# Kernel optimization log

Hardware: AMD Instinct MI355X
Metric: run time of the kernel (lower is better)

## Reference

```python
import jax, jax.numpy as jnp
import numpy as np

N_NODES = 100000
N_EDGES = 1600000
IN_DIM = 64
HID = 128
N_GRAPHS = 64
N_CLASSES = 2
EPS = 1e-5


def setup_inputs() -> dict:
    key = jax.random.key(0)
    ks = jax.random.split(key, 8)
    x = jax.random.normal(ks[0], (N_NODES, IN_DIM), dtype=jnp.float32)
    edge_index = jax.random.randint(ks[1], (2, N_EDGES), 0, N_NODES, dtype=jnp.int64)
    batch = jnp.sort(jax.random.randint(ks[2], (N_NODES,), 0, N_GRAPHS, dtype=jnp.int64))
    W1 = jax.random.normal(ks[3], (IN_DIM, HID), dtype=jnp.float32) / np.sqrt(IN_DIM)
    b1 = jnp.zeros((HID,), jnp.float32)
    W2 = jax.random.normal(ks[4], (HID, HID), dtype=jnp.float32) / np.sqrt(HID)
    b2 = jnp.zeros((HID,), jnp.float32)
    gamma = jnp.ones((HID,), jnp.float32)
    beta = jnp.zeros((HID,), jnp.float32)
    fcW = jax.random.normal(ks[5], (HID, N_CLASSES), dtype=jnp.float32) / np.sqrt(HID)
    fcb = jnp.zeros((N_CLASSES,), jnp.float32)
    return {"x": x, "edge_index": edge_index, "batch": batch, "W1": W1, "b1": b1,
            "W2": W2, "b2": b2, "gamma": gamma, "beta": beta, "fcW": fcW, "fcb": fcb}


def reference(x, edge_index, batch, W1, b1, W2, b2, gamma, beta, fcW, fcb):
    n = x.shape[0]
    loop = jnp.arange(n)
    # GCNConv adds self-loops and uses symmetric normalization D^-1/2 (A+I) D^-1/2
    src = jnp.concatenate([edge_index[0], loop])
    dst = jnp.concatenate([edge_index[1], loop])
    deg = jax.ops.segment_sum(jnp.ones_like(dst, dtype=x.dtype), dst, num_segments=n)
    dis = jax.lax.rsqrt(deg)  # deg >= 1 thanks to self-loops
    enorm = dis[src] * dis[dst]  # [E+N]

    def gcn(h, W, b):
        h = h @ W                                   # transform first (PyG order)
        msg = h[src] * enorm[:, None]               # gather + scale
        return jax.ops.segment_sum(msg, dst, num_segments=n) + b  # scatter-add

    cnt = jnp.maximum(jax.ops.segment_sum(jnp.ones((n,), x.dtype), batch,
                                          num_segments=N_GRAPHS), 1.0)[:, None]

    def inst_norm(h):
        # per-graph, per-channel normalization over nodes (affine=False)
        mean = jax.ops.segment_sum(h, batch, num_segments=N_GRAPHS) / cnt
        var = jax.ops.segment_sum(h * h, batch, num_segments=N_GRAPHS) / cnt - mean * mean
        return (h - mean[batch]) * jax.lax.rsqrt(var[batch] + EPS)

    h = jax.nn.relu(inst_norm(gcn(x, W1, b1)))   # dropout = identity (eval)
    h = jax.nn.relu(inst_norm(gcn(h, W2, b2)))
    pooled = jax.ops.segment_sum(h, batch, num_segments=N_GRAPHS) / cnt  # global mean pool
    # BatchNorm1d over the graph dimension (batch statistics, affine)
    m = jnp.mean(pooled, axis=0)
    v = jnp.mean((pooled - m) ** 2, axis=0)
    z = (pooled - m) * jax.lax.rsqrt(v + EPS) * gamma + beta
    return z @ fcW + fcb
```

## Files before the change

kernel.cpp:

```cpp
#include <hip/hip_runtime.h>
#include <hip/hip_bf16.h>


#define HID 128
#define NGRAPH 64
#define EPSN 1e-5f
#define BSHIFT 8
#define NBMAX 512

typedef unsigned int uint;
typedef unsigned short ushort;
typedef __attribute__((ext_vector_type(8))) short short8;
typedef __attribute__((ext_vector_type(4))) float f32x4;

static __device__ __forceinline__ ushort f2bf(float f) {
  uint x = __float_as_uint(f);
  return (ushort)((x + 0x7FFFu + ((x >> 16) & 1u)) >> 16);
}
static __device__ __forceinline__ float bf_lo(uint u) { return __uint_as_float(u << 16); }
static __device__ __forceinline__ float bf_hi(uint u) {
  return __uint_as_float(u & 0xFFFF0000u);
}

__global__ __launch_bounds__(256) void graph_starts(const int* __restrict__ batch,
                                                    int* __restrict__ gstart, int N) {
  int i = blockIdx.x * 256 + threadIdx.x;
  if (i >= N) return;
  int g = batch[i];
  if (i == 0) {
    for (int q = 0; q <= g; ++q) gstart[q] = 0;
  } else {
    int gp = batch[i - 1];
    if (g != gp)
      for (int q = gp + 1; q <= g; ++q) gstart[q] = i;
  }
  if (i == N - 1)
    for (int q = g + 1; q <= NGRAPH; ++q) gstart[q] = N;
}

__global__ __launch_bounds__(256) void bin_edges(const int* __restrict__ src,
                                                 const int* __restrict__ dst,
                                                 int* __restrict__ gcursor,
                                                 uint* __restrict__ records, int E, int NB,
                                                 int cap) {
  __shared__ int h[NBMAX];
  __shared__ int base[NBMAX];
  for (int i = threadIdx.x; i < NB; i += 256) h[i] = 0;
  __syncthreads();
  int e0 = blockIdx.x * 4096;
  int d[16], s[16];
#pragma unroll
  for (int k = 0; k < 16; ++k) {
    int e = e0 + k * 256 + threadIdx.x;
    if (e < E) {
      d[k] = dst[e];
      s[k] = src[e];
      atomicAdd(&h[d[k] >> BSHIFT], 1);
    }
  }
  __syncthreads();
  for (int i = threadIdx.x; i < NB; i += 256) {
    int c = h[i];
    if (c) base[i] = i * cap + atomicAdd(&gcursor[i], c);
  }
  __syncthreads();
  for (int i = threadIdx.x; i < NB; i += 256) h[i] = 0;
  __syncthreads();
#pragma unroll
  for (int k = 0; k < 16; ++k) {
    int e = e0 + k * 256 + threadIdx.x;
    if (e < E) {
      int b = d[k] >> BSHIFT;
      int lp = atomicAdd(&h[b], 1);
      records[base[b] + lp] = ((uint)s[k] << 8) | (uint)(d[k] & 255);
    }
  }
}

__global__ __launch_bounds__(256) void build_csr(const uint* __restrict__ records,
                                                 const int* __restrict__ gcursor,
                                                 int* __restrict__ row_beg,
                                                 int* __restrict__ row_end,
                                                 float* __restrict__ dis,
                                                 int* __restrict__ esrc, int N, int cap) {
  const int b = blockIdx.x;
  const int node0 = b << BSHIFT;
  const int nn = min(256, N - node0);
  const int beg = b * cap;
  const int cnt = gcursor[b];
  const int t = threadIdx.x;
  __shared__ int lc[256], sc[256], lcur[256];
  lc[t] = 0;
  __syncthreads();
  for (int i = t; i < cnt; i += 256) atomicAdd(&lc[records[beg + i] & 255u], 1);
  __syncthreads();
  int myc = lc[t];
  sc[t] = myc;
  __syncthreads();
  for (int off = 1; off < 256; off <<= 1) {
    int add = (t >= off) ? sc[t - off] : 0;
    __syncthreads();
    sc[t] += add;
    __syncthreads();
  }
  int excl = sc[t] - myc;
  if (t < nn) {
    row_beg[node0 + t] = beg + excl;
    row_end[node0 + t] = beg + excl + myc;
    dis[node0 + t] = rsqrtf((float)myc + 1.0f);
  }
  lcur[t] = excl;
  __syncthreads();
  for (int i = t; i < cnt; i += 256) {
    uint r = records[beg + i];
    int p = atomicAdd(&lcur[r & 255u], 1);
    esrc[beg + p] = (int)(r >> 8);
  }
}

__global__ __launch_bounds__(256) void xscale_bf16(const float* __restrict__ X,
                                                   const float* __restrict__ dis,
                                                   ushort* __restrict__ XS, int n4) {
  int i4 = blockIdx.x * 256 + threadIdx.x;
  if (i4 >= n4) return;
  int n = i4 >> 4;
  float dn = dis[n];
  float4 v = ((const float4*)X)[i4];
  ushort4 u;
  u.x = f2bf(v.x * dn);
  u.y = f2bf(v.y * dn);
  u.z = f2bf(v.z * dn);
  u.w = f2bf(v.w * dn);
  ((ushort4*)XS)[i4] = u;
}

__global__ __launch_bounds__(256) void wt_both(const float* __restrict__ W1,
                                               const float* __restrict__ W2,
                                               ushort* __restrict__ w1t,
                                               ushort* __restrict__ w2t) {
  int i = blockIdx.x * 256 + threadIdx.x;
  if (i < 128 * 64) {
    int c = i / 64, k = i - c * 64;
    w1t[i] = f2bf(W1[(size_t)k * HID + c]);
  } else {
    int i2 = i - 128 * 64;
    if (i2 < 128 * 128) {
      int c = i2 / 128, k = i2 - c * 128;
      w2t[i2] = f2bf(W2[(size_t)k * HID + c]);
    }
  }
}

__global__ __launch_bounds__(256) void aggregate64(const ushort* __restrict__ XS,
                                                   const int* __restrict__ row_beg,
                                                   const int* __restrict__ row_end,
                                                   const int* __restrict__ esrc,
                                                   const float* __restrict__ dis,
                                                   ushort* __restrict__ out, int N) {
  int wave = (int)((blockIdx.x * 256 + threadIdx.x) >> 6);
  const int l = threadIdx.x & 63;
  const int n = wave * 2 + (l >> 5);
  if (n >= N) return;
  const int j = l & 31;
  const float dn = dis[n];
  const int beg = row_beg[n];
  const int len = row_end[n] - beg;
  const uint* Xj = (const uint*)XS + j;
  float a0 = 0.f, a1 = 0.f, b0 = 0.f, b1 = 0.f;
  int i = 0;
  for (; i + 7 < len; i += 8) {
    int s0 = esrc[beg + i], s1 = esrc[beg + i + 1];
    int s2 = esrc[beg + i + 2], s3 = esrc[beg + i + 3];
    int s4 = esrc[beg + i + 4], s5 = esrc[beg + i + 5];
    int s6 = esrc[beg + i + 6], s7 = esrc[beg + i + 7];
    uint u0 = Xj[(size_t)s0 * 32];
    uint u1 = Xj[(size_t)s1 * 32];
    uint u2 = Xj[(size_t)s2 * 32];
    uint u3 = Xj[(size_t)s3 * 32];
    uint u4 = Xj[(size_t)s4 * 32];
    uint u5 = Xj[(size_t)s5 * 32];
    uint u6 = Xj[(size_t)s6 * 32];
    uint u7 = Xj[(size_t)s7 * 32];
    a0 += bf_lo(u0) + bf_lo(u1) + bf_lo(u2) + bf_lo(u3);
    a1 += bf_hi(u0) + bf_hi(u1) + bf_hi(u2) + bf_hi(u3);
    b0 += bf_lo(u4) + bf_lo(u5) + bf_lo(u6) + bf_lo(u7);
    b1 += bf_hi(u4) + bf_hi(u5) + bf_hi(u6) + bf_hi(u7);
  }
  for (; i < len; ++i) {
    uint u = Xj[(size_t)esrc[beg + i] * 32];
    a0 += bf_lo(u);
    a1 += bf_hi(u);
  }
  uint us = Xj[(size_t)n * 32];
  a0 += b0 + bf_lo(us);
  a1 += b1 + bf_hi(us);
  ((uint*)out)[(size_t)n * 32 + j] = (uint)f2bf(a0 * dn) | ((uint)f2bf(a1 * dn) << 16);
}

__global__ __launch_bounds__(256) void aggregate128(const ushort* __restrict__ H,
                                                    const int* __restrict__ row_beg,
                                                    const int* __restrict__ row_end,
                                                    const int* __restrict__ esrc,
                                                    const float* __restrict__ dis,
                                                    const float* __restrict__ bias,
                                                    ushort* __restrict__ outz, int N) {
  int wave = (int)((blockIdx.x * 256 + threadIdx.x) >> 6);
  const int l = threadIdx.x & 63;
  const int n = wave * 2 + (l >> 5);
  if (n >= N) return;
  const int j = l & 31;
  const float dn = dis[n];
  const int beg = row_beg[n];
  const int len = row_end[n] - beg;
  const uint2* Hj = (const uint2*)H + j;
  float a0 = 0.f, a1 = 0.f, a2 = 0.f, a3 = 0.f;
  float b0 = 0.f, b1 = 0.f, b2 = 0.f, b3 = 0.f;
  int i = 0;
  for (; i + 7 < len; i += 8) {
    int s0 = esrc[beg + i], s1 = esrc[beg + i + 1];
    int s2 = esrc[beg + i + 2], s3 = esrc[beg + i + 3];
    int s4 = esrc[beg + i + 4], s5 = esrc[beg + i + 5];
    int s6 = esrc[beg + i + 6], s7 = esrc[beg + i + 7];
    uint2 u0 = Hj[(size_t)s0 * 32];
    uint2 u1 = Hj[(size_t)s1 * 32];
    uint2 u2 = Hj[(size_t)s2 * 32];
    uint2 u3 = Hj[(size_t)s3 * 32];
    uint2 u4 = Hj[(size_t)s4 * 32];
    uint2 u5 = Hj[(size_t)s5 * 32];
    uint2 u6 = Hj[(size_t)s6 * 32];
    uint2 u7 = Hj[(size_t)s7 * 32];
    a0 += bf_lo(u0.x) + bf_lo(u1.x) + bf_lo(u2.x) + bf_lo(u3.x);
    a1 += bf_hi(u0.x) + bf_hi(u1.x) + bf_hi(u2.x) + bf_hi(u3.x);
    a2 += bf_lo(u0.y) + bf_lo(u1.y) + bf_lo(u2.y) + bf_lo(u3.y);
    a3 += bf_hi(u0.y) + bf_hi(u1.y) + bf_hi(u2.y) + bf_hi(u3.y);
    b0 += bf_lo(u4.x) + bf_lo(u5.x) + bf_lo(u6.x) + bf_lo(u7.x);
    b1 += bf_hi(u4.x) + bf_hi(u5.x) + bf_hi(u6.x) + bf_hi(u7.x);
    b2 += bf_lo(u4.y) + bf_lo(u5.y) + bf_lo(u6.y) + bf_lo(u7.y);
    b3 += bf_hi(u4.y) + bf_hi(u5.y) + bf_hi(u6.y) + bf_hi(u7.y);
  }
  for (; i < len; ++i) {
    uint2 u = Hj[(size_t)esrc[beg + i] * 32];
    a0 += bf_lo(u.x);
    a1 += bf_hi(u.x);
    a2 += bf_lo(u.y);
    a3 += bf_hi(u.y);
  }
  uint2 us = Hj[(size_t)n * 32];
  a0 += b0 + bf_lo(us.x);
  a1 += b1 + bf_hi(us.x);
  a2 += b2 + bf_lo(us.y);
  a3 += b3 + bf_hi(us.y);
  float4 bv = ((const float4*)bias)[j];
  uint2 o;
  o.x = (uint)f2bf(a0 * dn + bv.x) | ((uint)f2bf(a1 * dn + bv.y) << 16);
  o.y = (uint)f2bf(a2 * dn + bv.z) | ((uint)f2bf(a3 * dn + bv.w) << 16);
  ((uint2*)outz)[(size_t)n * 32 + j] = o;
}

template <int K, bool FUSE_NORM, bool DIS_SCALE, bool HAS_BIAS>
__global__ __launch_bounds__(256) void gemm_mfma(const ushort* __restrict__ X,
                                                 const ushort* __restrict__ Wt,
                                                 const float* __restrict__ bias,
                                                 const int* __restrict__ batch,
                                                 const float* __restrict__ mean,
                                                 const float* __restrict__ inv,
                                                 const float* __restrict__ disv,
                                                 ushort* __restrict__ Y, int N) {
  const int t = threadIdx.x;
  const int w = t >> 6;
  const int l = t & 63;
  const int lr = l & 15;
  const int lk = l >> 4;
  const int row0 = blockIdx.x * 64 + w * 16;
  const int arow = min(row0 + lr, N - 1);
  int g = 0;
  if (FUSE_NORM) g = batch[arow];
  f32x4 acc[8];
#pragma unroll
  for (int i = 0; i < 8; ++i) acc[i] = (f32x4){0.f, 0.f, 0.f, 0.f};
#pragma unroll
  for (int k0 = 0; k0 < K; k0 += 32) {
    const int kbase = k0 + lk * 8;
    short8 a = *(const short8*)(X + (size_t)arow * K + kbase);
    if (FUSE_NORM) {
      const float* mp = mean + g * HID + kbase;
      const float* ip = inv + g * HID + kbase;
      short8 an;
#pragma unroll
      for (int j = 0; j < 8; ++j) {
        float f = __uint_as_float((uint)(ushort)a[j] << 16);
        f = fmaxf((f - mp[j]) * ip[j], 0.f);
        an[j] = (short)f2bf(f);
      }
      a = an;
    }
#pragma unroll
    for (int nf = 0; nf < 8; ++nf) {
      short8 b = *(const short8*)(Wt + (size_t)(nf * 16 + lr) * K + kbase);
      acc[nf] = __builtin_amdgcn_mfma_f32_16x16x32_bf16(a, b, acc[nf], 0, 0, 0);
    }
  }
#pragma unroll
  for (int r = 0; r < 4; ++r) {
    int grow = row0 + lk * 4 + r;
    if (grow < N) {
      float ds = DIS_SCALE ? disv[grow] : 1.f;
#pragma unroll
      for (int nf = 0; nf < 8; ++nf) {
        int col = nf * 16 + lr;
        float v = acc[nf][r];
        if (HAS_BIAS) v += bias[col];
        v *= ds;
        Y[(size_t)grow * HID + col] = f2bf(v);
      }
    }
  }
}

__global__ __launch_bounds__(256) void stats_pass(const ushort* __restrict__ G,
                                                  const int* __restrict__ batch,
                                                  float* __restrict__ gsum,
                                                  float* __restrict__ gsq, int N) {
  const int c2 = threadIdx.x & 63;
  const int sub = threadIdx.x >> 6;
  const int n0 = blockIdx.x * 64 + sub * 16;
  const int n1 = min(n0 + 16, N);
  const uint* Gj = (const uint*)G + c2;
  float s0 = 0.f, s1 = 0.f, q0 = 0.f, q1 = 0.f;
  int cur = -1;
  for (int n = n0; n < n1; ++n) {
    int g = batch[n];
    if (g != cur) {
      if (cur >= 0) {
        atomicAdd(&gsum[cur * HID + 2 * c2], s0);
        atomicAdd(&gsum[cur * HID + 2 * c2 + 1], s1);
        atomicAdd(&gsq[cur * HID + 2 * c2], q0);
        atomicAdd(&gsq[cur * HID + 2 * c2 + 1], q1);
      }
      cur = g;
      s0 = s1 = q0 = q1 = 0.f;
    }
    uint u = Gj[(size_t)n * 64];
    float v0 = bf_lo(u), v1 = bf_hi(u);
    s0 += v0;
    s1 += v1;
    q0 += v0 * v0;
    q1 += v1 * v1;
  }
  if (cur >= 0) {
    atomicAdd(&gsum[cur * HID + 2 * c2], s0);
    atomicAdd(&gsum[cur * HID + 2 * c2 + 1], s1);
    atomicAdd(&gsq[cur * HID + 2 * c2], q0);
    atomicAdd(&gsq[cur * HID + 2 * c2 + 1], q1);
  }
}

__global__ __launch_bounds__(256) void finalize_stats(const float* __restrict__ gsum,
                                                      const float* __restrict__ gsq,
                                                      const int* __restrict__ gstart,
                                                      float* __restrict__ mean,
                                                      float* __restrict__ inv) {
  int i = blockIdx.x * 256 + threadIdx.x;
  if (i >= NGRAPH * HID) return;
  int g = i >> 7;
  float c = fmaxf((float)(gstart[g + 1] - gstart[g]), 1.f);
  float m = gsum[i] / c;
  float v = gsq[i] / c - m * m;
  mean[i] = m;
  inv[i] = rsqrtf(v + EPSN);
}

__global__ __launch_bounds__(256) void norm_relu_pool(const ushort* __restrict__ G,
                                                      const int* __restrict__ batch,
                                                      const float* __restrict__ mean,
                                                      const float* __restrict__ inv,
                                                      float* __restrict__ pooled, int N) {
  const int c2 = threadIdx.x & 63;
  const int sub = threadIdx.x >> 6;
  const int n0 = blockIdx.x * 64 + sub * 16;
  const int n1 = min(n0 + 16, N);
  const uint* Gj = (const uint*)G + c2;
  float p0 = 0.f, p1 = 0.f;
  int cur = -1;
  float2 mv = {0.f, 0.f}, iv = {0.f, 0.f};
  for (int n = n0; n < n1; ++n) {
    int g = batch[n];
    if (g != cur) {
      if (cur >= 0) {
        atomicAdd(&pooled[cur * HID + 2 * c2], p0);
        atomicAdd(&pooled[cur * HID + 2 * c2 + 1], p1);
      }
      cur = g;
      p0 = p1 = 0.f;
      mv = ((const float2*)mean)[g * 64 + c2];
      iv = ((const float2*)inv)[g * 64 + c2];
    }
    uint u = Gj[(size_t)n * 64];
    p0 += fmaxf((bf_lo(u) - mv.x) * iv.x, 0.f);
    p1 += fmaxf((bf_hi(u) - mv.y) * iv.y, 0.f);
  }
  if (cur >= 0) {
    atomicAdd(&pooled[cur * HID + 2 * c2], p0);
    atomicAdd(&pooled[cur * HID + 2 * c2 + 1], p1);
  }
}

__global__ __launch_bounds__(256) void final_head(const float* __restrict__ pooled_sum,
                                                  const int* __restrict__ gstart,
                                                  const float* __restrict__ gamma,
                                                  const float* __restrict__ beta,
                                                  const float* __restrict__ fcW,
                                                  const float* __restrict__ fcb,
                                                  float* __restrict__ out) {
  __shared__ float P[NGRAPH][HID];
  __shared__ float zs[HID], zb[HID];
  int t = threadIdx.x;
  for (int i = t; i < NGRAPH * HID; i += 256) {
    int g = i >> 7;
    float c = fmaxf((float)(gstart[g + 1] - gstart[g]), 1.f);
    P[g][i & 127] = pooled_sum[i] / c;
  }
  __syncthreads();
  if (t < HID) {
    float m = 0.f;
    for (int g = 0; g < NGRAPH; ++g) m += P[g][t];
    m *= (1.f / NGRAPH);
    float v = 0.f;
    for (int g = 0; g < NGRAPH; ++g) {
      float d = P[g][t] - m;
      v += d * d;
    }
    v *= (1.f / NGRAPH);
    float sc = rsqrtf(v + EPSN) * gamma[t];
    zs[t] = sc;
    zb[t] = beta[t] - m * sc;
  }
  __syncthreads();
  if (t < NGRAPH * 2) {
    int g = t >> 1, k = t & 1;
    float acc = fcb[k];
    for (int c = 0; c < HID; ++c) {
      float z = P[g][c] * zs[c] + zb[c];
      acc += z * fcW[c * 2 + k];
    }
    out[t] = acc;
  }
}

extern "C" void kernel_launch(void* const* d_in, const int* in_sizes, int n_in,
                              void* d_out, int out_size, void* d_ws, size_t ws_size,
                              hipStream_t stream) {
  const float* x = (const float*)d_in[0];
  const int* ei = (const int*)d_in[1];
  const int* batch = (const int*)d_in[2];
  const float* W1 = (const float*)d_in[3];
  const float* b1 = (const float*)d_in[4];
  const float* W2 = (const float*)d_in[5];
  const float* b2 = (const float*)d_in[6];
  const float* gamma = (const float*)d_in[7];
  const float* beta = (const float*)d_in[8];
  const float* fcW = (const float*)d_in[9];
  const float* fcb = (const float*)d_in[10];
  float* out = (float*)d_out;

  const int N = in_sizes[2];
  const int E = in_sizes[1] / 2;
  const int* srcp = ei;
  const int* dstp = ei + E;
  const int NB = (N + 255) >> BSHIFT;
  const int cap = 2 * (E / NB) + 256;

  float* ws = (float*)d_ws;
  size_t off = 0;
  auto alloc = [&](size_t n) {
    float* p = ws + off;
    off += (n + 127) & ~(size_t)127;
    return p;
  };
  int* row_beg = (int*)alloc(N);
  int* row_end = (int*)alloc(N);
  int* esrc = (int*)alloc((size_t)NB * cap);
  size_t recsz = ((size_t)NB * cap > (size_t)N * 32 ? (size_t)NB * cap : (size_t)N * 32);
  float* recbuf = alloc(recsz);
  float* dis = alloc(N);
  float* y1b = alloc((size_t)N * 32);
  float* h1b = alloc((size_t)N * 64);
  float* h2b = alloc((size_t)N * 64);
  float* zb_ = alloc((size_t)N * 64);
  float* w1tb = alloc(128 * 64 / 2);
  float* w2tb = alloc(128 * 128 / 2);
  int* gstart = (int*)alloc(NGRAPH + 1);
  float* zero0 = ws + off;
  int* gcursor = (int*)alloc(NBMAX);
  float* gsum1 = alloc(NGRAPH * HID);
  float* gsq1 = alloc(NGRAPH * HID);
  float* gsum2 = alloc(NGRAPH * HID);
  float* gsq2 = alloc(NGRAPH * HID);
  float* pooled = alloc(NGRAPH * HID);
  size_t zero_bytes = (size_t)((ws + off) - zero0) * sizeof(float);
  float* mean1 = alloc(NGRAPH * HID);
  float* inv1 = alloc(NGRAPH * HID);
  float* mean2 = alloc(NGRAPH * HID);
  float* inv2 = alloc(NGRAPH * HID);

  uint* records = (uint*)recbuf;
  ushort* xs = (ushort*)recbuf;
  ushort* y1 = (ushort*)y1b;
  ushort* h1 = (ushort*)h1b;
  ushort* h2s = (ushort*)h2b;
  ushort* z = (ushort*)zb_;
  ushort* w1t = (ushort*)w1tb;
  ushort* w2t = (ushort*)w2tb;

  const int nblkN = (N + 255) / 256;
  const int nblkE4k = (E + 4095) / 4096;

  hipMemsetAsync(zero0, 0, zero_bytes, stream);

  wt_both<<<(128 * 64 + 128 * 128 + 255) / 256, 256, 0, stream>>>(W1, W2, w1t, w2t);
  graph_starts<<<nblkN, 256, 0, stream>>>(batch, gstart, N);
  bin_edges<<<nblkE4k, 256, 0, stream>>>(srcp, dstp, gcursor, records, E, NB, cap);
  build_csr<<<NB, 256, 0, stream>>>(records, gcursor, row_beg, row_end, dis, esrc, N, cap);

  const int aggBlocks = ((N + 1) / 2 + 3) / 4;
  const int gemmBlocks = (N + 63) / 64;
  const int nrmBlocks = (N + 63) / 64;

  xscale_bf16<<<(N * 16 + 255) / 256, 256, 0, stream>>>(x, dis, xs, N * 16);
  aggregate64<<<aggBlocks, 256, 0, stream>>>(xs, row_beg, row_end, esrc, dis, y1, N);
  gemm_mfma<64, false, false, true><<<gemmBlocks, 256, 0, stream>>>(
      y1, w1t, b1, nullptr, nullptr, nullptr, nullptr, h1, N);
  stats_pass<<<nrmBlocks, 256, 0, stream>>>(h1, batch, gsum1, gsq1, N);
  finalize_stats<<<(NGRAPH * HID + 255) / 256, 256, 0, stream>>>(gsum1, gsq1, gstart, mean1, inv1);

  gemm_mfma<128, true, true, false><<<gemmBlocks, 256, 0, stream>>>(
      h1, w2t, nullptr, batch, mean1, inv1, dis, h2s, N);
  aggregate128<<<aggBlocks, 256, 0, stream>>>(h2s, row_beg, row_end, esrc, dis, b2, z, N);
  stats_pass<<<nrmBlocks, 256, 0, stream>>>(z, batch, gsum2, gsq2, N);
  finalize_stats<<<(NGRAPH * HID + 255) / 256, 256, 0, stream>>>(gsum2, gsq2, gstart, mean2, inv2);
  norm_relu_pool<<<nrmBlocks, 256, 0, stream>>>(z, batch, mean2, inv2, pooled, N);

  final_head<<<1, 256, 0, stream>>>(pooled, gstart, gamma, beta, fcW, fcb, out);
}
```

Measured before the change: 302.6 us.

## Split aggregation feature columns across block pairs and replicate stat accumulators

The two aggregation kernels now give each node's feature row to two blocks, each covering half the columns with 16 lanes per node. That spreads gather traffic over more blocks and narrows the per-lane access footprint. Separately, the per-graph sum, sum-of-squares and pooling accumulators are replicated four ways by block index, which cuts atomic contention on the same addresses. The finalize and head kernels then sum the four replicas. In exchange, each node's edge list is walked twice, once per column half, and slightly more memory must be zeroed.

```diff
diff --git a/kernel.cpp b/kernel.cpp
--- a/kernel.cpp
+++ b/kernel.cpp
@@ -7,6 +7,8 @@
 #define EPSN 1e-5f
 #define BSHIFT 8
 #define NBMAX 512
+#define REP 4
+#define NH (NGRAPH * HID)
 
 typedef unsigned int uint;
 typedef unsigned short ushort;
@@ -16,6 +18,9 @@
 static __device__ __forceinline__ ushort f2bf(float f) {
   uint x = __float_as_uint(f);
   return (ushort)((x + 0x7FFFu + ((x >> 16) & 1u)) >> 16);
+}
+static __device__ __forceinline__ uint pack2(float a, float b) {
+  return (uint)f2bf(a) | ((uint)f2bf(b) << 16);
 }
 static __device__ __forceinline__ float bf_lo(uint u) { return __uint_as_float(u << 16); }
 static __device__ __forceinline__ float bf_hi(uint u) {
@@ -157,15 +162,17 @@
                                                    const int* __restrict__ esrc,
                                                    const float* __restrict__ dis,
                                                    ushort* __restrict__ out, int N) {
-  int wave = (int)((blockIdx.x * 256 + threadIdx.x) >> 6);
+  const int slice = blockIdx.x & 1;
+  const int nb = blockIdx.x >> 1;
   const int l = threadIdx.x & 63;
-  const int n = wave * 2 + (l >> 5);
+  const int w = threadIdx.x >> 6;
+  const int n = nb * 16 + w * 4 + (l >> 4);
   if (n >= N) return;
-  const int j = l & 31;
+  const int j = l & 15;
   const float dn = dis[n];
   const int beg = row_beg[n];
   const int len = row_end[n] - beg;
-  const uint* Xj = (const uint*)XS + j;
+  const uint* Xj = (const uint*)XS + slice * 16 + j;
   float a0 = 0.f, a1 = 0.f, b0 = 0.f, b1 = 0.f;
   int i = 0;
   for (; i + 7 < len; i += 8) {
@@ -194,7 +201,7 @@
   uint us = Xj[(size_t)n * 32];
   a0 += b0 + bf_lo(us);
   a1 += b1 + bf_hi(us);
-  ((uint*)out)[(size_t)n * 32 + j] = (uint)f2bf(a0 * dn) | ((uint)f2bf(a1 * dn) << 16);
+  ((uint*)out)[(size_t)n * 32 + slice * 16 + j] = pack2(a0 * dn, a1 * dn);
 }
 
 __global__ __launch_bounds__(256) void aggregate128(const ushort* __restrict__ H,
@@ -204,15 +211,17 @@
                                                     const float* __restrict__ dis,
                                                     const float* __restrict__ bias,
                                                     ushort* __restrict__ outz, int N) {
-  int wave = (int)((blockIdx.x * 256 + threadIdx.x) >> 6);
+  const int slice = blockIdx.x & 1;
+  const int nb = blockIdx.x >> 1;
   const int l = threadIdx.x & 63;
-  const int n = wave * 2 + (l >> 5);
+  const int w = threadIdx.x >> 6;
+  const int n = nb * 16 + w * 4 + (l >> 4);
   if (n >= N) return;
-  const int j = l & 31;
+  const int j = l & 15;
   const float dn = dis[n];
   const int beg = row_beg[n];
   const int len = row_end[n] - beg;
-  const uint2* Hj = (const uint2*)H + j;
+  const uint2* Hj = (const uint2*)H + slice * 16 + j;
   float a0 = 0.f, a1 = 0.f, a2 = 0.f, a3 = 0.f;
   float b0 = 0.f, b1 = 0.f, b2 = 0.f, b3 = 0.f;
   int i = 0;
@@ -250,11 +259,11 @@
   a1 += b1 + bf_hi(us.x);
   a2 += b2 + bf_lo(us.y);
   a3 += b3 + bf_hi(us.y);
-  float4 bv = ((const float4*)bias)[j];
+  float4 bv = ((const float4*)bias)[slice * 16 + j];
   uint2 o;
-  o.x = (uint)f2bf(a0 * dn + bv.x) | ((uint)f2bf(a1 * dn + bv.y) << 16);
-  o.y = (uint)f2bf(a2 * dn + bv.z) | ((uint)f2bf(a3 * dn + bv.w) << 16);
-  ((uint2*)outz)[(size_t)n * 32 + j] = o;
+  o.x = pack2(a0 * dn + bv.x, a1 * dn + bv.y);
+  o.y = pack2(a2 * dn + bv.z, a3 * dn + bv.w);
+  ((uint2*)outz)[(size_t)n * 32 + slice * 16 + j] = o;
 }
 
 template <int K, bool FUSE_NORM, bool DIS_SCALE, bool HAS_BIAS>
@@ -325,6 +334,9 @@
   const int sub = threadIdx.x >> 6;
   const int n0 = blockIdx.x * 64 + sub * 16;
   const int n1 = min(n0 + 16, N);
+  const int roff = (blockIdx.x & (REP - 1)) * NH;
+  float* gs = gsum + roff;
+  float* gq = gsq + roff;
   const uint* Gj = (const uint*)G + c2;
   float s0 = 0.f, s1 = 0.f, q0 = 0.f, q1 = 0.f;
   int cur = -1;
@@ -332,10 +344,10 @@
     int g = batch[n];
     if (g != cur) {
       if (cur >= 0) {
-        atomicAdd(&gsum[cur * HID + 2 * c2], s0);
-        atomicAdd(&gsum[cur * HID + 2 * c2 + 1], s1);
-        atomicAdd(&gsq[cur * HID + 2 * c2], q0);
-        atomicAdd(&gsq[cur * HID + 2 * c2 + 1], q1);
+        atomicAdd(&gs[cur * HID + 2 * c2], s0);
+        atomicAdd(&gs[cur * HID + 2 * c2 + 1], s1);
+        atomicAdd(&gq[cur * HID + 2 * c2], q0);
+        atomicAdd(&gq[cur * HID + 2 * c2 + 1], q1);
       }
       cur = g;
       s0 = s1 = q0 = q1 = 0.f;
@@ -348,10 +360,10 @@
     q1 += v1 * v1;
   }
   if (cur >= 0) {
-    atomicAdd(&gsum[cur * HID + 2 * c2], s0);
-    atomicAdd(&gsum[cur * HID + 2 * c2 + 1], s1);
-    atomicAdd(&gsq[cur * HID + 2 * c2], q0);
-    atomicAdd(&gsq[cur * HID + 2 * c2 + 1], q1);
+    atomicAdd(&gs[cur * HID + 2 * c2], s0);
+    atomicAdd(&gs[cur * HID + 2 * c2 + 1], s1);
+    atomicAdd(&gq[cur * HID + 2 * c2], q0);
+    atomicAdd(&gq[cur * HID + 2 * c2 + 1], q1);
   }
 }
 
@@ -361,11 +373,13 @@
                                                       float* __restrict__ mean,
                                                       float* __restrict__ inv) {
   int i = blockIdx.x * 256 + threadIdx.x;
-  if (i >= NGRAPH * HID) return;
+  if (i >= NH) return;
   int g = i >> 7;
   float c = fmaxf((float)(gstart[g + 1] - gstart[g]), 1.f);
-  float m = gsum[i] / c;
-  float v = gsq[i] / c - m * m;
+  float s = gsum[i] + gsum[i + NH] + gsum[i + 2 * NH] + gsum[i + 3 * NH];
+  float q = gsq[i] + gsq[i + NH] + gsq[i + 2 * NH] + gsq[i + 3 * NH];
+  float m = s / c;
+  float v = q / c - m * m;
   mean[i] = m;
   inv[i] = rsqrtf(v + EPSN);
 }
@@ -379,6 +393,7 @@
   const int sub = threadIdx.x >> 6;
   const int n0 = blockIdx.x * 64 + sub * 16;
   const int n1 = min(n0 + 16, N);
+  float* pl = pooled + (blockIdx.x & (REP - 1)) * NH;
   const uint* Gj = (const uint*)G + c2;
   float p0 = 0.f, p1 = 0.f;
   int cur = -1;
@@ -387,8 +402,8 @@
     int g = batch[n];
     if (g != cur) {
       if (cur >= 0) {
-        atomicAdd(&pooled[cur * HID + 2 * c2], p0);
-        atomicAdd(&pooled[cur * HID + 2 * c2 + 1], p1);
+        atomicAdd(&pl[cur * HID + 2 * c2], p0);
+        atomicAdd(&pl[cur * HID + 2 * c2 + 1], p1);
       }
       cur = g;
       p0 = p1 = 0.f;
@@ -400,8 +415,8 @@
     p1 += fmaxf((bf_hi(u) - mv.y) * iv.y, 0.f);
   }
   if (cur >= 0) {
-    atomicAdd(&pooled[cur * HID + 2 * c2], p0);
-    atomicAdd(&pooled[cur * HID + 2 * c2 + 1], p1);
+    atomicAdd(&pl[cur * HID + 2 * c2], p0);
+    atomicAdd(&pl[cur * HID + 2 * c2 + 1], p1);
   }
 }
 
@@ -415,10 +430,12 @@
   __shared__ float P[NGRAPH][HID];
   __shared__ float zs[HID], zb[HID];
   int t = threadIdx.x;
-  for (int i = t; i < NGRAPH * HID; i += 256) {
+  for (int i = t; i < NH; i += 256) {
     int g = i >> 7;
     float c = fmaxf((float)(gstart[g + 1] - gstart[g]), 1.f);
-    P[g][i & 127] = pooled_sum[i] / c;
+    float s = pooled_sum[i] + pooled_sum[i + NH] + pooled_sum[i + 2 * NH] +
+              pooled_sum[i + 3 * NH];
+    P[g][i & 127] = s / c;
   }
   __syncthreads();
   if (t < HID) {
@@ -492,16 +509,16 @@
   int* gstart = (int*)alloc(NGRAPH + 1);
   float* zero0 = ws + off;
   int* gcursor = (int*)alloc(NBMAX);
-  float* gsum1 = alloc(NGRAPH * HID);
-  float* gsq1 = alloc(NGRAPH * HID);
-  float* gsum2 = alloc(NGRAPH * HID);
-  float* gsq2 = alloc(NGRAPH * HID);
-  float* pooled = alloc(NGRAPH * HID);
+  float* gsum1 = alloc(NH * REP);
+  float* gsq1 = alloc(NH * REP);
+  float* gsum2 = alloc(NH * REP);
+  float* gsq2 = alloc(NH * REP);
+  float* pooled = alloc(NH * REP);
   size_t zero_bytes = (size_t)((ws + off) - zero0) * sizeof(float);
-  float* mean1 = alloc(NGRAPH * HID);
-  float* inv1 = alloc(NGRAPH * HID);
-  float* mean2 = alloc(NGRAPH * HID);
-  float* inv2 = alloc(NGRAPH * HID);
+  float* mean1 = alloc(NH);
+  float* inv1 = alloc(NH);
+  float* mean2 = alloc(NH);
+  float* inv2 = alloc(NH);
 
   uint* records = (uint*)recbuf;
   ushort* xs = (ushort*)recbuf;
@@ -522,7 +539,7 @@
   bin_edges<<<nblkE4k, 256, 0, stream>>>(srcp, dstp, gcursor, records, E, NB, cap);
   build_csr<<<NB, 256, 0, stream>>>(records, gcursor, row_beg, row_end, dis, esrc, N, cap);
 
-  const int aggBlocks = ((N + 1) / 2 + 3) / 4;
+  const int aggBlocks = 2 * ((N + 15) / 16);
   const int gemmBlocks = (N + 63) / 64;
   const int nrmBlocks = (N + 63) / 64;
 
@@ -531,13 +548,13 @@
   gemm_mfma<64, false, false, true><<<gemmBlocks, 256, 0, stream>>>(
       y1, w1t, b1, nullptr, nullptr, nullptr, nullptr, h1, N);
   stats_pass<<<nrmBlocks, 256, 0, stream>>>(h1, batch, gsum1, gsq1, N);
-  finalize_stats<<<(NGRAPH * HID + 255) / 256, 256, 0, stream>>>(gsum1, gsq1, gstart, mean1, inv1);
+  finalize_stats<<<(NH + 255) / 256, 256, 0, stream>>>(gsum1, gsq1, gstart, mean1, inv1);
 
   gemm_mfma<128, true, true, false><<<gemmBlocks, 256, 0, stream>>>(
       h1, w2t, nullptr, batch, mean1, inv1, dis, h2s, N);
   aggregate128<<<aggBlocks, 256, 0, stream>>>(h2s, row_beg, row_end, esrc, dis, b2, z, N);
   stats_pass<<<nrmBlocks, 256, 0, stream>>>(z, batch, gsum2, gsq2, N);
-  finalize_stats<<<(NGRAPH * HID + 255) / 256, 256, 0, stream>>>(gsum2, gsq2, gstart, mean2, inv2);
+  finalize_stats<<<(NH + 255) / 256, 256, 0, stream>>>(gsum2, gsq2, gstart, mean2, inv2);
   norm_relu_pool<<<nrmBlocks, 256, 0, stream>>>(z, batch, mean2, inv2, pooled, N);
 
   final_head<<<1, 256, 0, stream>>>(pooled, gstart, gamma, beta, fcW, fcb, out);
```

Result: slower. 317.8 us (+5.0%).
